# Optimization experiments

Hardware: AMD Instinct MI355X
Metric: run time of the kernel (lower is better)

## Reference

```python
import jax, jax.numpy as jnp
import numpy as np

N, D, K = 32768, 128, 16
EPS = 1e-8  # torch cosine_similarity eps


def setup_inputs() -> dict:
    key = jax.random.key(0)
    k1, k2, kW1, kW2, kV = jax.random.split(key, 5)
    # xavier_normal std for [K, fan_in, fan_out]-style tensors (torch treats dim0 as batch? no:
    # xavier_normal_ on a 3D tensor uses fan_in = D*1? torch computes fan from dims 1.. with receptive field.
    # fan_in = size(1)*rf, fan_out = size(0)*rf where rf = prod(shape[2:]).
    def xavier_std(shape):
        rf = int(np.prod(shape[2:])) if len(shape) > 2 else 1
        fan_in = shape[1] * rf
        fan_out = shape[0] * rf
        return float(np.sqrt(2.0 / (fan_in + fan_out)))
    W1 = jax.random.normal(kW1, (K, D, D), jnp.float32) * xavier_std((K, D, D))
    W2 = jax.random.normal(kW2, (K, D, D), jnp.float32) * xavier_std((K, D, D))
    V = jax.random.normal(kV, (K, 2 * D, 1), jnp.float32) * xavier_std((K, 2 * D, 1))
    b = jnp.zeros((K,), jnp.float32)
    x_1 = jax.random.normal(k1, (N, D), jnp.float32)
    x_2 = jax.random.normal(k2, (N, D), jnp.float32)
    return {"x_1": x_1, "x_2": x_2, "W1": W1, "W2": W2, "V": V, "b": b}


def reference(x_1, x_2, W1, W2, V, b):
    # Batched version of the per-slice loop: one bmm per side instead of K matmuls.
    x1_t = jnp.einsum('nd,kde->kne', x_1, W1)  # [K, N, D]
    x2_t = jnp.einsum('nd,kde->kne', x_2, W2)  # [K, N, D]
    # torch.cosine_similarity(dim=-1): dot / (clamp(||a||, eps) * clamp(||b||, eps))
    num = jnp.sum(x1_t * x2_t, axis=-1)                      # [K, N]
    n1 = jnp.maximum(jnp.sqrt(jnp.sum(x1_t * x1_t, -1)), EPS)
    n2 = jnp.maximum(jnp.sqrt(jnp.sum(x2_t * x2_t, -1)), EPS)
    part1 = num / (n1 * n2)                                  # [K, N]
    x_cat = jnp.concatenate([x_1, x_2], axis=-1)             # [N, 2D]
    part2 = jnp.einsum('nc,kc->kn', x_cat, V[:, :, 0])       # [K, N]
    fea = part1 + part2 + b[:, None]                         # [K, N]
    return jax.nn.relu(fea.T)                                # [N, K]
```

## Files before the change

kernel.cpp:

```cpp
#include <hip/hip_runtime.h>


typedef __attribute__((ext_vector_type(8))) __bf16 bf16x8;
typedef __attribute__((ext_vector_type(8))) unsigned short us8;
typedef __attribute__((ext_vector_type(4))) float f32x4;

static __device__ __forceinline__ unsigned short f2bf(float f) {
  unsigned u = __float_as_uint(f);
  u += 0x7FFFu + ((u >> 16) & 1u);
  return (unsigned short)(u >> 16);
}

static __device__ __forceinline__ bf16x8 as_bf(us8 u) {
  bf16x8 r;
  __builtin_memcpy(&r, &u, sizeof(r));
  return r;
}

__global__ void ntn_prep(const float* __restrict__ W1, const float* __restrict__ W2,
                         const float* __restrict__ V,
                         unsigned short* __restrict__ wsW, unsigned short* __restrict__ wsV) {
  int e2 = blockIdx.x * 256 + threadIdx.x;
  if (e2 < 524288) {
    int j = e2 & 7, t = e2 >> 3;
    int u = t & 2047, cc = t >> 11;
    int lane = u & 63, s = (u >> 6) & 3, et2 = (u >> 8) & 3, side = (u >> 10) & 1;
    int h = cc & 1, k = cc >> 1;
    int q = lane >> 4, l15 = lane & 15;
    int et = h * 4 + et2;
    const float* W = side ? W2 : W1;
    wsW[e2] = f2bf(W[k * 16384 + (s * 32 + q * 8 + j) * 128 + (et * 16 + l15)]);
  } else if (e2 < 528384) {
    int v2 = e2 - 524288;
    int j = v2 & 7, u = v2 >> 3;
    int lane = u & 63, cs = u >> 6;
    int q = lane >> 4, l15 = lane & 15;
    wsV[v2] = f2bf(V[l15 * 256 + cs * 32 + q * 8 + j]);
  }
}

__global__ __launch_bounds__(256, 2) void ntn_main(
    const float* __restrict__ x1, const float* __restrict__ x2,
    const float* __restrict__ b,
    const unsigned short* __restrict__ wsW, const unsigned short* __restrict__ wsV,
    float* __restrict__ out) {
  __shared__ uint4 ldsW[2][2048];

  const int tid = threadIdx.x;
  const int lane = tid & 63, wave = tid >> 6;
  const int q = lane >> 4, l15 = lane & 15;
  const int kh = blockIdx.x & 1;
  const int rb = blockIdx.x >> 1;
  const int rowbase = rb * 128 + wave * 32;

  const f32x4 zero4 = {0.f, 0.f, 0.f, 0.f};

  auto stage = [&](int cc, int slot) {
    const unsigned short* src = wsW + (size_t)cc * 16384 + (size_t)(wave * 512 + lane) * 8;
    uint4* dst = &ldsW[slot][wave * 512];
#pragma unroll
    for (int i = 0; i < 8; ++i)
      __builtin_amdgcn_global_load_lds(
          (__attribute__((address_space(1))) void*)(void*)(src + i * 512),
          (__attribute__((address_space(3))) void*)(dst + i * 64), 16, 0, 0);
  };

  stage(kh * 16, 0);

  bf16x8 xb[2][2][4];
#pragma unroll
  for (int side = 0; side < 2; ++side) {
    const float* xp0 = side ? x2 : x1;
#pragma unroll
    for (int nt = 0; nt < 2; ++nt) {
#pragma unroll
      for (int s = 0; s < 4; ++s) {
        const float* p = xp0 + (size_t)(rowbase + nt * 16 + l15) * 128 + s * 32 + q * 8;
        float4 v0 = *(const float4*)p;
        float4 v1 = *(const float4*)(p + 4);
        us8 uu;
        uu[0] = f2bf(v0.x); uu[1] = f2bf(v0.y); uu[2] = f2bf(v0.z); uu[3] = f2bf(v0.w);
        uu[4] = f2bf(v1.x); uu[5] = f2bf(v1.y); uu[6] = f2bf(v1.z); uu[7] = f2bf(v1.w);
        xb[side][nt][s] = as_bf(uu);
      }
    }
  }

  f32x4 accP[2];
  {
    bf16x8 vf[8];
#pragma unroll
    for (int cs = 0; cs < 8; ++cs)
      vf[cs] = as_bf(*(const us8*)(wsV + (size_t)(cs * 64 + lane) * 8));
    float4 bv = *(const float4*)(b + q * 4);
#pragma unroll
    for (int nt = 0; nt < 2; ++nt) {
      f32x4 a = zero4;
#pragma unroll
      for (int cs = 0; cs < 8; ++cs)
        a = __builtin_amdgcn_mfma_f32_16x16x32_bf16(vf[cs], xb[cs >> 2][nt][cs & 3], a, 0, 0, 0);
      a.x += bv.x; a.y += bv.y; a.z += bv.z; a.w += bv.w;
      accP[nt] = a;
    }
  }

  float nm[2] = {0.f, 0.f}, q1[2] = {0.f, 0.f}, q2[2] = {0.f, 0.f};

  auto compute = [&](int slot) {
#pragma unroll
    for (int et = 0; et < 4; ++et) {
      bf16x8 wa[4], wb[4];
#pragma unroll
      for (int s = 0; s < 4; ++s) {
        wa[s] = as_bf(*(const us8*)&ldsW[slot][et * 256 + s * 64 + lane]);
        wb[s] = as_bf(*(const us8*)&ldsW[slot][1024 + et * 256 + s * 64 + lane]);
      }
#pragma unroll
      for (int nt = 0; nt < 2; ++nt) {
        f32x4 a1 = zero4, a2 = zero4;
#pragma unroll
        for (int s = 0; s < 4; ++s)
          a1 = __builtin_amdgcn_mfma_f32_16x16x32_bf16(wa[s], xb[0][nt][s], a1, 0, 0, 0);
#pragma unroll
        for (int s = 0; s < 4; ++s)
          a2 = __builtin_amdgcn_mfma_f32_16x16x32_bf16(wb[s], xb[1][nt][s], a2, 0, 0, 0);
        nm[nt] += a1.x * a2.x + a1.y * a2.y + a1.z * a2.z + a1.w * a2.w;
        q1[nt] += a1.x * a1.x + a1.y * a1.y + a1.z * a1.z + a1.w * a1.w;
        q2[nt] += a2.x * a2.x + a2.y * a2.y + a2.z * a2.z + a2.w * a2.w;
      }
    }
  };

#pragma unroll 1
  for (int kk = 0; kk < 8; ++kk) {
    const int cbase = kh * 16 + 2 * kk;
    __syncthreads();
    stage(cbase + 1, 1);
    compute(0);
    __syncthreads();
    if (kk < 7) stage(cbase + 2, 0);
    compute(1);

    const int k = kh * 8 + kk;
    const int qo = k >> 2;
    const int r  = k & 3;
#pragma unroll
    for (int nt = 0; nt < 2; ++nt) {
      float n = nm[nt], s1 = q1[nt], s2 = q2[nt];
      n  += __shfl_xor(n, 16);  n  += __shfl_xor(n, 32);
      s1 += __shfl_xor(s1, 16); s1 += __shfl_xor(s1, 32);
      s2 += __shfl_xor(s2, 16); s2 += __shfl_xor(s2, 32);
      float d1 = fmaxf(sqrtf(s1), 1e-8f);
      float d2 = fmaxf(sqrtf(s2), 1e-8f);
      float p1 = n / (d1 * d2);
      float pc = (r == 0) ? accP[nt].x : (r == 1) ? accP[nt].y
               : (r == 2) ? accP[nt].z : accP[nt].w;
      if (q == qo)
        out[(size_t)(rowbase + nt * 16 + l15) * 16 + k] = fmaxf(p1 + pc, 0.f);
      nm[nt] = 0.f; q1[nt] = 0.f; q2[nt] = 0.f;
    }
  }
}

extern "C" void kernel_launch(void* const* d_in, const int* in_sizes, int n_in,
                              void* d_out, int out_size, void* d_ws, size_t ws_size,
                              hipStream_t stream) {
  const float* x1 = (const float*)d_in[0];
  const float* x2 = (const float*)d_in[1];
  const float* W1 = (const float*)d_in[2];
  const float* W2 = (const float*)d_in[3];
  const float* V  = (const float*)d_in[4];
  const float* b  = (const float*)d_in[5];
  float* out = (float*)d_out;
  unsigned short* wsW = (unsigned short*)d_ws;
  unsigned short* wsV = wsW + (size_t)65536 * 8;

  ntn_prep<<<2064, 256, 0, stream>>>(W1, W2, V, wsW, wsV);
  ntn_main<<<512, 256, 0, stream>>>(x1, x2, b, wsW, wsV, out);
}
```

Baseline: 119.4 us.

## Switch MFMA tiles from 16x16x32 to 32x32x16 with matching weight layout

Changes the bf16 matrix products from 16x16x32 MFMA to 32x32x16 MFMA, so each wave covers its 32 rows with one 32-row tile instead of two 16-row tiles. The prep kernel re-packs W1/W2 and V, with V padded to 32 rows of zeros, to match the new operand layout, and the reductions and output indexing are rewritten. The larger instruction should cut instruction count and LDS fragment reloads per useful FLOP, but the 16-wide accumulators raise register use, so launch bounds drop to one block per SIMD, which reduces occupancy. The V projection now does wasted work on the zero-padded rows.

```diff
diff --git a/kernel.cpp b/kernel.cpp
--- a/kernel.cpp
+++ b/kernel.cpp
@@ -3,7 +3,7 @@
 
 typedef __attribute__((ext_vector_type(8))) __bf16 bf16x8;
 typedef __attribute__((ext_vector_type(8))) unsigned short us8;
-typedef __attribute__((ext_vector_type(4))) float f32x4;
+typedef __attribute__((ext_vector_type(16))) float f32x16;
 
 static __device__ __forceinline__ unsigned short f2bf(float f) {
   unsigned u = __float_as_uint(f);
@@ -22,24 +22,27 @@
                          unsigned short* __restrict__ wsW, unsigned short* __restrict__ wsV) {
   int e2 = blockIdx.x * 256 + threadIdx.x;
   if (e2 < 524288) {
-    int j = e2 & 7, t = e2 >> 3;
-    int u = t & 2047, cc = t >> 11;
-    int lane = u & 63, s = (u >> 6) & 3, et2 = (u >> 8) & 3, side = (u >> 10) & 1;
+    int j = e2 & 7, tu = e2 >> 3;
+    int u = tu & 2047, cc = tu >> 11;
+    int lane = u & 63, s = (u >> 6) & 7, t = (u >> 9) & 1, side = (u >> 10) & 1;
     int h = cc & 1, k = cc >> 1;
-    int q = lane >> 4, l15 = lane & 15;
-    int et = h * 4 + et2;
+    int l31 = lane & 31, g = lane >> 5;
+    int d = s * 16 + g * 8 + j;
+    int e = (h * 2 + t) * 32 + l31;
     const float* W = side ? W2 : W1;
-    wsW[e2] = f2bf(W[k * 16384 + (s * 32 + q * 8 + j) * 128 + (et * 16 + l15)]);
-  } else if (e2 < 528384) {
+    wsW[e2] = f2bf(W[k * 16384 + d * 128 + e]);
+  } else if (e2 < 524288 + 8192) {
     int v2 = e2 - 524288;
     int j = v2 & 7, u = v2 >> 3;
-    int lane = u & 63, cs = u >> 6;
-    int q = lane >> 4, l15 = lane & 15;
-    wsV[v2] = f2bf(V[l15 * 256 + cs * 32 + q * 8 + j]);
+    int lane = u & 63, cs2 = u >> 6;
+    int l31 = lane & 31, g = lane >> 5;
+    int c = cs2 * 16 + g * 8 + j;
+    float val = (l31 < 16) ? V[l31 * 256 + c] : 0.f;
+    wsV[v2] = f2bf(val);
   }
 }
 
-__global__ __launch_bounds__(256, 2) void ntn_main(
+__global__ __launch_bounds__(256, 1) void ntn_main(
     const float* __restrict__ x1, const float* __restrict__ x2,
     const float* __restrict__ b,
     const unsigned short* __restrict__ wsW, const unsigned short* __restrict__ wsV,
@@ -48,12 +51,12 @@
 
   const int tid = threadIdx.x;
   const int lane = tid & 63, wave = tid >> 6;
-  const int q = lane >> 4, l15 = lane & 15;
+  const int l31 = lane & 31, g = lane >> 5;
   const int kh = blockIdx.x & 1;
   const int rb = blockIdx.x >> 1;
   const int rowbase = rb * 128 + wave * 32;
 
-  const f32x4 zero4 = {0.f, 0.f, 0.f, 0.f};
+  const f32x16 zero16 = {0.f,0.f,0.f,0.f,0.f,0.f,0.f,0.f,0.f,0.f,0.f,0.f,0.f,0.f,0.f,0.f};
 
   auto stage = [&](int cc, int slot) {
     const unsigned short* src = wsW + (size_t)cc * 16384 + (size_t)(wave * 512 + lane) * 8;
@@ -67,66 +70,58 @@
 
   stage(kh * 16, 0);
 
-  bf16x8 xb[2][2][4];
+  bf16x8 xb[2][8];
 #pragma unroll
   for (int side = 0; side < 2; ++side) {
     const float* xp0 = side ? x2 : x1;
 #pragma unroll
-    for (int nt = 0; nt < 2; ++nt) {
-#pragma unroll
-      for (int s = 0; s < 4; ++s) {
-        const float* p = xp0 + (size_t)(rowbase + nt * 16 + l15) * 128 + s * 32 + q * 8;
-        float4 v0 = *(const float4*)p;
-        float4 v1 = *(const float4*)(p + 4);
-        us8 uu;
-        uu[0] = f2bf(v0.x); uu[1] = f2bf(v0.y); uu[2] = f2bf(v0.z); uu[3] = f2bf(v0.w);
-        uu[4] = f2bf(v1.x); uu[5] = f2bf(v1.y); uu[6] = f2bf(v1.z); uu[7] = f2bf(v1.w);
-        xb[side][nt][s] = as_bf(uu);
-      }
+    for (int s = 0; s < 8; ++s) {
+      const float* p = xp0 + (size_t)(rowbase + l31) * 128 + s * 16 + g * 8;
+      float4 v0 = *(const float4*)p;
+      float4 v1 = *(const float4*)(p + 4);
+      us8 uu;
+      uu[0] = f2bf(v0.x); uu[1] = f2bf(v0.y); uu[2] = f2bf(v0.z); uu[3] = f2bf(v0.w);
+      uu[4] = f2bf(v1.x); uu[5] = f2bf(v1.y); uu[6] = f2bf(v1.z); uu[7] = f2bf(v1.w);
+      xb[side][s] = as_bf(uu);
     }
   }
 
-  f32x4 accP[2];
+  float accP[8];
   {
-    bf16x8 vf[8];
+    f32x16 a = zero16;
 #pragma unroll
-    for (int cs = 0; cs < 8; ++cs)
-      vf[cs] = as_bf(*(const us8*)(wsV + (size_t)(cs * 64 + lane) * 8));
-    float4 bv = *(const float4*)(b + q * 4);
+    for (int cs2 = 0; cs2 < 16; ++cs2) {
+      bf16x8 vf = as_bf(*(const us8*)(wsV + (size_t)(cs2 * 64 + lane) * 8));
+      a = __builtin_amdgcn_mfma_f32_32x32x16_bf16(vf, xb[cs2 >> 3][cs2 & 7], a, 0, 0, 0);
+    }
 #pragma unroll
-    for (int nt = 0; nt < 2; ++nt) {
-      f32x4 a = zero4;
-#pragma unroll
-      for (int cs = 0; cs < 8; ++cs)
-        a = __builtin_amdgcn_mfma_f32_16x16x32_bf16(vf[cs], xb[cs >> 2][nt][cs & 3], a, 0, 0, 0);
-      a.x += bv.x; a.y += bv.y; a.z += bv.z; a.w += bv.w;
-      accP[nt] = a;
-    }
+    for (int r = 0; r < 8; ++r)
+      accP[r] = a[r] + b[(r & 3) + 8 * ((r >> 2) & 1) + 4 * g];
   }
 
-  float nm[2] = {0.f, 0.f}, q1[2] = {0.f, 0.f}, q2[2] = {0.f, 0.f};
+  float nm = 0.f, q1 = 0.f, q2 = 0.f;
 
   auto compute = [&](int slot) {
 #pragma unroll
-    for (int et = 0; et < 4; ++et) {
-      bf16x8 wa[4], wb[4];
+    for (int t = 0; t < 2; ++t) {
+      bf16x8 wa[8], wb[8];
 #pragma unroll
-      for (int s = 0; s < 4; ++s) {
-        wa[s] = as_bf(*(const us8*)&ldsW[slot][et * 256 + s * 64 + lane]);
-        wb[s] = as_bf(*(const us8*)&ldsW[slot][1024 + et * 256 + s * 64 + lane]);
+      for (int s = 0; s < 8; ++s) {
+        wa[s] = as_bf(*(const us8*)&ldsW[slot][t * 512 + s * 64 + lane]);
+        wb[s] = as_bf(*(const us8*)&ldsW[slot][1024 + t * 512 + s * 64 + lane]);
       }
+      f32x16 a1 = zero16, a2 = zero16;
 #pragma unroll
-      for (int nt = 0; nt < 2; ++nt) {
-        f32x4 a1 = zero4, a2 = zero4;
+      for (int s = 0; s < 8; ++s)
+        a1 = __builtin_amdgcn_mfma_f32_32x32x16_bf16(wa[s], xb[0][s], a1, 0, 0, 0);
 #pragma unroll
-        for (int s = 0; s < 4; ++s)
-          a1 = __builtin_amdgcn_mfma_f32_16x16x32_bf16(wa[s], xb[0][nt][s], a1, 0, 0, 0);
+      for (int s = 0; s < 8; ++s)
+        a2 = __builtin_amdgcn_mfma_f32_32x32x16_bf16(wb[s], xb[1][s], a2, 0, 0, 0);
 #pragma unroll
-        for (int s = 0; s < 4; ++s)
-          a2 = __builtin_amdgcn_mfma_f32_16x16x32_bf16(wb[s], xb[1][nt][s], a2, 0, 0, 0);
-        nm[nt] += a1.x * a2.x + a1.y * a2.y + a1.z * a2.z + a1.w * a2.w;
-        q1[nt] += a1.x * a1.x + a1.y * a1.y + a1.z * a1.z + a1.w * a1.w;
-        q2[nt] += a2.x * a2.x + a2.y * a2.y + a2.z * a2.z + a2.w * a2.w;
+      for (int r = 0; r < 16; ++r) {
+        nm += a1[r] * a2[r];
+        q1 += a1[r] * a1[r];
+        q2 += a2[r] * a2[r];
       }
     }
   };
@@ -142,23 +137,20 @@
     compute(1);
 
     const int k = kh * 8 + kk;
-    const int qo = k >> 2;
-    const int r  = k & 3;
-#pragma unroll
-    for (int nt = 0; nt < 2; ++nt) {
-      float n = nm[nt], s1 = q1[nt], s2 = q2[nt];
-      n  += __shfl_xor(n, 16);  n  += __shfl_xor(n, 32);
-      s1 += __shfl_xor(s1, 16); s1 += __shfl_xor(s1, 32);
-      s2 += __shfl_xor(s2, 16); s2 += __shfl_xor(s2, 32);
-      float d1 = fmaxf(sqrtf(s1), 1e-8f);
-      float d2 = fmaxf(sqrtf(s2), 1e-8f);
-      float p1 = n / (d1 * d2);
-      float pc = (r == 0) ? accP[nt].x : (r == 1) ? accP[nt].y
-               : (r == 2) ? accP[nt].z : accP[nt].w;
-      if (q == qo)
-        out[(size_t)(rowbase + nt * 16 + l15) * 16 + k] = fmaxf(p1 + pc, 0.f);
-      nm[nt] = 0.f; q1[nt] = 0.f; q2[nt] = 0.f;
-    }
+    float n = nm, s1 = q1, s2 = q2;
+    n  += __shfl_xor(n, 32);
+    s1 += __shfl_xor(s1, 32);
+    s2 += __shfl_xor(s2, 32);
+    float d1 = fmaxf(sqrtf(s1), 1e-8f);
+    float d2 = fmaxf(sqrtf(s2), 1e-8f);
+    float p1 = n / (d1 * d2);
+    int rr = (k & 3) | ((k >> 1) & 4);
+    float pc = rr == 0 ? accP[0] : rr == 1 ? accP[1] : rr == 2 ? accP[2]
+             : rr == 3 ? accP[3] : rr == 4 ? accP[4] : rr == 5 ? accP[5]
+             : rr == 6 ? accP[6] : accP[7];
+    if (g == ((k >> 2) & 1))
+      out[(size_t)(rowbase + l31) * 16 + k] = fmaxf(p1 + pc, 0.f);
+    nm = 0.f; q1 = 0.f; q2 = 0.f;
   }
 }
 
@@ -175,6 +167,6 @@
   unsigned short* wsW = (unsigned short*)d_ws;
   unsigned short* wsV = wsW + (size_t)65536 * 8;
 
-  ntn_prep<<<2064, 256, 0, stream>>>(W1, W2, V, wsW, wsV);
+  ntn_prep<<<2080, 256, 0, stream>>>(W1, W2, V, wsW, wsV);
   ntn_main<<<512, 256, 0, stream>>>(x1, x2, b, wsW, wsV, out);
 }
```

After: 130.6 us. +9.3%, slower.

## Load weight fragments directly from global into registers, dropping LDS staging

Applied to the files above, without the earlier changes.

Removes the LDS double-buffer and its __syncthreads barriers. Each wave now loads bf16 weight fragments straight from global memory (L2-cached) into a 4-deep register ring, prefetching two fragments ahead of the MFMA work. Launch bounds drop to one block per SIMD pair to make room for the extra registers. This trades shared-memory reuse across the block's four waves for more global/L2 traffic and lower occupancy, while avoiding barrier stalls.

```diff
diff --git a/kernel.cpp b/kernel.cpp
--- a/kernel.cpp
+++ b/kernel.cpp
@@ -39,13 +39,11 @@
   }
 }
 
-__global__ __launch_bounds__(256, 2) void ntn_main(
+__global__ __launch_bounds__(256, 1) void ntn_main(
     const float* __restrict__ x1, const float* __restrict__ x2,
     const float* __restrict__ b,
     const unsigned short* __restrict__ wsW, const unsigned short* __restrict__ wsV,
     float* __restrict__ out) {
-  __shared__ uint4 ldsW[2][2048];
-
   const int tid = threadIdx.x;
   const int lane = tid & 63, wave = tid >> 6;
   const int q = lane >> 4, l15 = lane & 15;
@@ -54,18 +52,6 @@
   const int rowbase = rb * 128 + wave * 32;
 
   const f32x4 zero4 = {0.f, 0.f, 0.f, 0.f};
-
-  auto stage = [&](int cc, int slot) {
-    const unsigned short* src = wsW + (size_t)cc * 16384 + (size_t)(wave * 512 + lane) * 8;
-    uint4* dst = &ldsW[slot][wave * 512];
-#pragma unroll
-    for (int i = 0; i < 8; ++i)
-      __builtin_amdgcn_global_load_lds(
-          (__attribute__((address_space(1))) void*)(void*)(src + i * 512),
-          (__attribute__((address_space(3))) void*)(dst + i * 64), 16, 0, 0);
-  };
-
-  stage(kh * 16, 0);
 
   bf16x8 xb[2][2][4];
 #pragma unroll
@@ -104,42 +90,50 @@
     }
   }
 
+  bf16x8 wra[4][4], wrb[4][4];
+  const us8* wsu = (const us8*)wsW;
+
+  auto loadfg = [&](int slot, int cc, int et) {
+    const us8* base = wsu + (size_t)cc * 2048 + et * 256 + lane;
+#pragma unroll
+    for (int s = 0; s < 4; ++s) wra[slot][s] = as_bf(base[s * 64]);
+#pragma unroll
+    for (int s = 0; s < 4; ++s) wrb[slot][s] = as_bf(base[1024 + s * 64]);
+  };
+
   float nm[2] = {0.f, 0.f}, q1[2] = {0.f, 0.f}, q2[2] = {0.f, 0.f};
 
   auto compute = [&](int slot) {
 #pragma unroll
-    for (int et = 0; et < 4; ++et) {
-      bf16x8 wa[4], wb[4];
+    for (int nt = 0; nt < 2; ++nt) {
+      f32x4 a1 = zero4, a2 = zero4;
 #pragma unroll
-      for (int s = 0; s < 4; ++s) {
-        wa[s] = as_bf(*(const us8*)&ldsW[slot][et * 256 + s * 64 + lane]);
-        wb[s] = as_bf(*(const us8*)&ldsW[slot][1024 + et * 256 + s * 64 + lane]);
-      }
+      for (int s = 0; s < 4; ++s)
+        a1 = __builtin_amdgcn_mfma_f32_16x16x32_bf16(wra[slot][s], xb[0][nt][s], a1, 0, 0, 0);
 #pragma unroll
-      for (int nt = 0; nt < 2; ++nt) {
-        f32x4 a1 = zero4, a2 = zero4;
-#pragma unroll
-        for (int s = 0; s < 4; ++s)
-          a1 = __builtin_amdgcn_mfma_f32_16x16x32_bf16(wa[s], xb[0][nt][s], a1, 0, 0, 0);
-#pragma unroll
-        for (int s = 0; s < 4; ++s)
-          a2 = __builtin_amdgcn_mfma_f32_16x16x32_bf16(wb[s], xb[1][nt][s], a2, 0, 0, 0);
-        nm[nt] += a1.x * a2.x + a1.y * a2.y + a1.z * a2.z + a1.w * a2.w;
-        q1[nt] += a1.x * a1.x + a1.y * a1.y + a1.z * a1.z + a1.w * a1.w;
-        q2[nt] += a2.x * a2.x + a2.y * a2.y + a2.z * a2.z + a2.w * a2.w;
-      }
+      for (int s = 0; s < 4; ++s)
+        a2 = __builtin_amdgcn_mfma_f32_16x16x32_bf16(wrb[slot][s], xb[1][nt][s], a2, 0, 0, 0);
+      nm[nt] += a1.x * a2.x + a1.y * a2.y + a1.z * a2.z + a1.w * a2.w;
+      q1[nt] += a1.x * a1.x + a1.y * a1.y + a1.z * a1.z + a1.w * a1.w;
+      q2[nt] += a2.x * a2.x + a2.y * a2.y + a2.z * a2.z + a2.w * a2.w;
     }
   };
 
+  loadfg(0, kh * 16 + 0, 0);
+  loadfg(1, kh * 16 + 0, 1);
+
 #pragma unroll 1
   for (int kk = 0; kk < 8; ++kk) {
-    const int cbase = kh * 16 + 2 * kk;
-    __syncthreads();
-    stage(cbase + 1, 1);
-    compute(0);
-    __syncthreads();
-    if (kk < 7) stage(cbase + 2, 0);
-    compute(1);
+#pragma unroll
+    for (int i = 0; i < 8; ++i) {
+      const int nf = kk * 8 + i + 2;
+      if (nf < 64) {
+        const int ni = nf & 7;
+        const int cc = kh * 16 + (nf >> 3) * 2 + (ni >> 2);
+        loadfg((i + 2) & 3, cc, ni & 3);
+      }
+      compute(i & 3);
+    }
 
     const int k = kh * 8 + kk;
     const int qo = k >> 2;
```

Measured after the change: 138.3 us. 15.8% more time.

## Split output-column tiles across wave pairs and double grid size

Applied to the files above, without the earlier changes.

Each block now covers 64 rows instead of 128. Pairs of waves split the 8 output-column tiles of each k slice between them, and the partial dot and norm sums are combined through a small shared-memory scratch buffer. The final cosine computation for each slice is deferred to just after the next barrier. The grid doubles to 1024 blocks, which gives more parallelism and halves per-wave MFMA work. In exchange, every block stages the same weights for half as many rows, and there is extra LDS traffic for the reduction.

```diff
diff --git a/kernel.cpp b/kernel.cpp
--- a/kernel.cpp
+++ b/kernel.cpp
@@ -45,13 +45,16 @@
     const unsigned short* __restrict__ wsW, const unsigned short* __restrict__ wsV,
     float* __restrict__ out) {
   __shared__ uint4 ldsW[2][2048];
+  __shared__ float scr[2][64][9];
 
   const int tid = threadIdx.x;
   const int lane = tid & 63, wave = tid >> 6;
   const int q = lane >> 4, l15 = lane & 15;
+  const int rw = wave >> 1;
+  const int eh = wave & 1;
   const int kh = blockIdx.x & 1;
   const int rb = blockIdx.x >> 1;
-  const int rowbase = rb * 128 + wave * 32;
+  const int rowbase = rb * 64 + rw * 32;
 
   const f32x4 zero4 = {0.f, 0.f, 0.f, 0.f};
 
@@ -108,7 +111,8 @@
 
   auto compute = [&](int slot) {
 #pragma unroll
-    for (int et = 0; et < 4; ++et) {
+    for (int e2 = 0; e2 < 2; ++e2) {
+      const int et = eh * 2 + e2;
       bf16x8 wa[4], wb[4];
 #pragma unroll
       for (int s = 0; s < 4; ++s) {
@@ -131,35 +135,60 @@
     }
   };
 
+  auto foldk = [&]() {
+#pragma unroll
+    for (int nt = 0; nt < 2; ++nt) {
+      float n = nm[nt], s1 = q1[nt], s2 = q2[nt];
+      n  += __shfl_xor(n, 16);  n  += __shfl_xor(n, 32);
+      s1 += __shfl_xor(s1, 16); s1 += __shfl_xor(s1, 32);
+      s2 += __shfl_xor(s2, 16); s2 += __shfl_xor(s2, 32);
+      if (eh == 1) {
+        scr[rw][lane][nt * 3 + 0] = n;
+        scr[rw][lane][nt * 3 + 1] = s1;
+        scr[rw][lane][nt * 3 + 2] = s2;
+        nm[nt] = 0.f; q1[nt] = 0.f; q2[nt] = 0.f;
+      } else {
+        nm[nt] = n; q1[nt] = s1; q2[nt] = s2;
+      }
+    }
+  };
+
+  auto finishk = [&](int kkp) {
+    if (eh == 0) {
+      const int k = kh * 8 + kkp;
+      const int qo = k >> 2;
+      const int r  = k & 3;
+#pragma unroll
+      for (int nt = 0; nt < 2; ++nt) {
+        float n  = nm[nt] + scr[rw][lane][nt * 3 + 0];
+        float s1 = q1[nt] + scr[rw][lane][nt * 3 + 1];
+        float s2 = q2[nt] + scr[rw][lane][nt * 3 + 2];
+        float d1 = fmaxf(sqrtf(s1), 1e-8f);
+        float d2 = fmaxf(sqrtf(s2), 1e-8f);
+        float p1 = n / (d1 * d2);
+        float pc = (r == 0) ? accP[nt].x : (r == 1) ? accP[nt].y
+                 : (r == 2) ? accP[nt].z : accP[nt].w;
+        if (q == qo)
+          out[(size_t)(rowbase + nt * 16 + l15) * 16 + k] = fmaxf(p1 + pc, 0.f);
+        nm[nt] = 0.f; q1[nt] = 0.f; q2[nt] = 0.f;
+      }
+    }
+  };
+
 #pragma unroll 1
   for (int kk = 0; kk < 8; ++kk) {
     const int cbase = kh * 16 + 2 * kk;
     __syncthreads();
+    if (kk > 0) finishk(kk - 1);
     stage(cbase + 1, 1);
     compute(0);
     __syncthreads();
     if (kk < 7) stage(cbase + 2, 0);
     compute(1);
-
-    const int k = kh * 8 + kk;
-    const int qo = k >> 2;
-    const int r  = k & 3;
-#pragma unroll
-    for (int nt = 0; nt < 2; ++nt) {
-      float n = nm[nt], s1 = q1[nt], s2 = q2[nt];
-      n  += __shfl_xor(n, 16);  n  += __shfl_xor(n, 32);
-      s1 += __shfl_xor(s1, 16); s1 += __shfl_xor(s1, 32);
-      s2 += __shfl_xor(s2, 16); s2 += __shfl_xor(s2, 32);
-      float d1 = fmaxf(sqrtf(s1), 1e-8f);
-      float d2 = fmaxf(sqrtf(s2), 1e-8f);
-      float p1 = n / (d1 * d2);
-      float pc = (r == 0) ? accP[nt].x : (r == 1) ? accP[nt].y
-               : (r == 2) ? accP[nt].z : accP[nt].w;
-      if (q == qo)
-        out[(size_t)(rowbase + nt * 16 + l15) * 16 + k] = fmaxf(p1 + pc, 0.f);
-      nm[nt] = 0.f; q1[nt] = 0.f; q2[nt] = 0.f;
-    }
-  }
+    foldk();
+  }
+  __syncthreads();
+  finishk(7);
 }
 
 extern "C" void kernel_launch(void* const* d_in, const int* in_sizes, int n_in,
@@ -176,5 +205,5 @@
   unsigned short* wsV = wsW + (size_t)65536 * 8;
 
   ntn_prep<<<2064, 256, 0, stream>>>(W1, W2, V, wsW, wsV);
-  ntn_main<<<512, 256, 0, stream>>>(x1, x2, b, wsW, wsV, out);
-}
+  ntn_main<<<1024, 256, 0, stream>>>(x1, x2, b, wsW, wsV, out);
+}
```

After: 137.5 us. +15.1%, slower.
